# Kernel tuning notes

Hardware: AMD Instinct MI355X
Metric: run time of the kernel (lower is better)

Reference implementation:

```python
import jax, jax.numpy as jnp
import numpy as np

D_IN = 1024
D_OUT = 1024
NUM_HEADS = 16
HEAD_DIM = D_OUT // NUM_HEADS


def setup_inputs() -> dict:
    key = jax.random.key(0)
    k1, k2, k3, k4 = jax.random.split(key, 4)
    x = jax.random.normal(k1, (2, 2048, D_IN), dtype=jnp.float32)
    # qkv Linear (bias=False): weight [3*d_out, d_in]
    w_qkv = jax.random.normal(k2, (3 * D_OUT, D_IN), dtype=jnp.float32) * (1.0 / np.sqrt(D_IN))
    # proj Linear (default bias=True): weight [d_out, d_out], bias [d_out]
    w_proj = jax.random.normal(k3, (D_OUT, D_OUT), dtype=jnp.float32) * (1.0 / np.sqrt(D_OUT))
    b_proj = jax.random.normal(k4, (D_OUT,), dtype=jnp.float32) * 0.01
    return {"x": x, "w_qkv": w_qkv, "w_proj": w_proj, "b_proj": b_proj}


def reference(x, w_qkv, w_proj, b_proj):
    B, S, E = x.shape
    qkv = jnp.einsum("bse,fe->bsf", x, w_qkv)                 # [B,S,3*d_out]
    qkv = qkv.reshape(B, S, 3, NUM_HEADS, HEAD_DIM)
    qkv = jnp.transpose(qkv, (2, 0, 3, 1, 4))                  # [3,B,H,S,D]
    q, k, v = qkv[0], qkv[1], qkv[2]
    scores = jnp.einsum("bhqd,bhkd->bhqk", q, k)               # [B,H,S,S]
    causal = jnp.triu(jnp.ones((S, S), dtype=bool), k=1)
    scores = jnp.where(causal, -jnp.inf, scores)
    # NOTE: source divides by head_dim**(-0.5), i.e. multiplies by sqrt(head_dim)
    scores = scores / (HEAD_DIM ** -0.5)
    attn = jax.nn.softmax(scores, axis=-1)
    ctx = jnp.einsum("bhqk,bhkd->bhqd", attn, v)               # [B,H,S,D]
    ctx = jnp.transpose(ctx, (0, 2, 1, 3)).reshape(B, S, E)
    return jnp.einsum("bse,fe->bsf", ctx, w_proj) + b_proj
```

## Files before the change

### kernel.cpp

```cpp
#include <hip/hip_runtime.h>

typedef _Float16 f16;
typedef _Float16 f16x4 __attribute__((ext_vector_type(4)));
typedef _Float16 f16x8 __attribute__((ext_vector_type(8)));
typedef float f32x4 __attribute__((ext_vector_type(4)));

#define MFMA16(a, b, c) __builtin_amdgcn_mfma_f32_16x16x32_f16(a, b, c, 0, 0, 0)
#define QSCALE 11.5415603f

typedef const __attribute__((address_space(1))) void* gp1_t;
typedef __attribute__((address_space(3))) void* lp3_t;
__device__ __forceinline__ void gld16(const void* g, void* l) {
    __builtin_amdgcn_global_load_lds((gp1_t)g, (lp3_t)l, 16, 0, 0);
}

__global__ __launch_bounds__(256) void cvt_all(
    const float* __restrict__ x, const float* __restrict__ wq, const float* __restrict__ wp,
    f16* __restrict__ xh, f16* __restrict__ wqh, f16* __restrict__ wph)
{
    int i = blockIdx.x * 256 + threadIdx.x;
    const float4* src; f16x4* dst; int off;
    if (i < 1048576)      { src = (const float4*)x;  dst = (f16x4*)xh;  off = i; }
    else if (i < 1835008) { src = (const float4*)wq; dst = (f16x4*)wqh; off = i - 1048576; }
    else                  { src = (const float4*)wp; dst = (f16x4*)wph; off = i - 1835008; }
    float4 v = src[off];
    f16x4 o = { (f16)v.x, (f16)v.y, (f16)v.z, (f16)v.w };
    dst[off] = o;
}

template<int EPI>
__global__ __launch_bounds__(256) void gemm_k(
    const f16* __restrict__ A, const f16* __restrict__ B, int K,
    f16* __restrict__ qb, f16* __restrict__ kb, f16* __restrict__ vt,
    float* __restrict__ outF, const float* __restrict__ bias)
{
    __shared__ f16 as[128 * 32];
    __shared__ f16 bs[128 * 32];
    const int t = threadIdx.x;
    const int m0 = blockIdx.y * 128, n0 = blockIdx.x * 128;
    const int lane = t & 63, wv = t >> 6;
    const int wm = wv >> 1, wn = wv & 1;
    const int lr = lane & 15, g = lane >> 4;
    const int srow = lane >> 2, schk = (lane & 3) * 8;
    const f16* Ab = A + (size_t)m0 * K;
    const f16* Bb = B + (size_t)n0 * K;
    f32x4 acc[4][4] = {};

    for (int k0 = 0; k0 < K; k0 += 32) {
        __syncthreads();
        #pragma unroll
        for (int i2 = 0; i2 < 2; ++i2) {
            const int r0 = wv * 32 + i2 * 16;
            gld16(&Ab[(size_t)(r0 + srow) * K + k0 + schk], &as[r0 * 32]);
            gld16(&Bb[(size_t)(r0 + srow) * K + k0 + schk], &bs[r0 * 32]);
        }
        __syncthreads();
        f16x8 af[4], bf[4];
        #pragma unroll
        for (int mt = 0; mt < 4; ++mt)
            af[mt] = *reinterpret_cast<const f16x8*>(&as[(wm * 64 + mt * 16 + lr) * 32 + g * 8]);
        #pragma unroll
        for (int nt = 0; nt < 4; ++nt)
            bf[nt] = *reinterpret_cast<const f16x8*>(&bs[(wn * 64 + nt * 16 + lr) * 32 + g * 8]);
        #pragma unroll
        for (int mt = 0; mt < 4; ++mt)
            #pragma unroll
            for (int nt = 0; nt < 4; ++nt)
                acc[mt][nt] = MFMA16(af[mt], bf[nt], acc[mt][nt]);
    }

    #pragma unroll
    for (int mt = 0; mt < 4; ++mt) {
        #pragma unroll
        for (int nt = 0; nt < 4; ++nt) {
            const int n = n0 + wn * 64 + nt * 16 + lr;
            const int s0 = m0 + wm * 64 + mt * 16 + 4 * g;
            if (EPI == 0) {
                const int which = n >> 10, h = (n >> 6) & 15, d = n & 63;
                const int b = s0 >> 11, s = s0 & 2047;
                if (which == 2) {
                    f16x4 vv;
                    #pragma unroll
                    for (int i = 0; i < 4; ++i) vv[i] = (f16)acc[mt][nt][i];
                    *reinterpret_cast<f16x4*>(&vt[((size_t)((b << 4) + h) * 64 + d) * 2048 + s]) = vv;
                } else {
                    f16* dst = which ? kb : qb;
                    const float sc = which ? 1.0f : QSCALE;
                    #pragma unroll
                    for (int i = 0; i < 4; ++i)
                        dst[((size_t)((b << 4) + h) * 2048 + (s + i)) * 64 + d] = (f16)(acc[mt][nt][i] * sc);
                }
            } else {
                #pragma unroll
                for (int i = 0; i < 4; ++i)
                    outF[(size_t)(s0 + i) * 1024 + n] = acc[mt][nt][i] + bias[n];
            }
        }
    }
}

__global__ __launch_bounds__(64, 2) void attn_k(
    const f16* __restrict__ Q, const f16* __restrict__ K, const f16* __restrict__ VT,
    f16* __restrict__ ctx, f16* __restrict__ opart,
    float* __restrict__ mpart, float* __restrict__ lpart)
{
    __shared__ f16 lp[64][72];
    const int lane = threadIdx.x;
    const int lr = lane & 15, g = lane >> 4;
    const int bid = blockIdx.x;
    const int bh = bid & 31;
    const int rr = 67 - (bid >> 5);
    int u, c;
    if (rr < 10)      { u = rr;                 c = 0; }
    else if (rr < 30) { u = 10 + (rr - 10) / 2; c = (rr - 10) % 2; }
    else if (rr < 60) { u = 20 + (rr - 30) / 3; c = (rr - 30) % 3; }
    else              { u = 30 + (rr - 60) / 4; c = (rr - 60) % 4; }
    const int ntt = u + 1;
    const int nc  = 1 + u / 10;
    const int cbase = ntt / nc, crem = ntt % nc;
    const int start = c * cbase + (c < crem ? c : crem);
    const int len   = cbase + (c < crem ? 1 : 0);
    const bool diag = (start + len == ntt);

    const int b = bh >> 4, h = bh & 15;
    const size_t base = (size_t)bh * (2048 * 64);
    const f16* Qb = Q + base;
    const f16* Kb = K + base;
    const f16* Vb = VT + base;
    const int q0 = u << 6;

    f16x8 qf[4][2];
    #pragma unroll
    for (int nt = 0; nt < 4; ++nt)
        #pragma unroll
        for (int ks = 0; ks < 2; ++ks)
            qf[nt][ks] = *reinterpret_cast<const f16x8*>(&Qb[(size_t)(q0 + nt * 16 + lr) * 64 + ks * 32 + g * 8]);

    f32x4 o[4][4] = {};
    float mrun[4] = { -1e30f, -1e30f, -1e30f, -1e30f };
    float lsum[4] = { 0.f, 0.f, 0.f, 0.f };

#define ATTN_TILE(KV0, DIAGM) do {                                                      \
    const int kv0_ = (KV0);                                                             \
    f32x4 st[4][4] = {};                                                                \
    _Pragma("unroll")                                                                   \
    for (int mt = 0; mt < 4; ++mt) {                                                    \
        f16x8 ak[2];                                                                    \
        _Pragma("unroll")                                                               \
        for (int ks = 0; ks < 2; ++ks)                                                  \
            ak[ks] = *reinterpret_cast<const f16x8*>(                                   \
                &Kb[(size_t)(kv0_ + mt * 16 + lr) * 64 + ks * 32 + g * 8]);             \
        _Pragma("unroll")                                                               \
        for (int nt = 0; nt < 4; ++nt)                                                  \
            if (!(DIAGM) || mt <= nt) {                                                 \
                _Pragma("unroll")                                                       \
                for (int ks = 0; ks < 2; ++ks)                                          \
                    st[mt][nt] = MFMA16(ak[ks], qf[nt][ks], st[mt][nt]);                \
            }                                                                           \
    }                                                                                   \
    _Pragma("unroll")                                                                   \
    for (int nt = 0; nt < 4; ++nt) {                                                    \
        float mloc = -1e30f;                                                            \
        _Pragma("unroll")                                                               \
        for (int mt = 0; mt < 4; ++mt) {                                                \
            if ((DIAGM) && mt > nt) continue;                                           \
            _Pragma("unroll")                                                           \
            for (int i = 0; i < 4; ++i) {                                               \
                float sv = st[mt][nt][i];                                               \
                if ((DIAGM) && mt == nt) {             \
                    sv = (4 * g + i <= lr) ? sv : -1e30f;                               \
                    st[mt][nt][i] = sv;                                                 \
                }                                                                       \
                mloc = fmaxf(mloc, sv);                                                 \
            }                                                                           \
        }                                                                               \
        mloc = fmaxf(mloc, __shfl_xor(mloc, 16));                                       \
        mloc = fmaxf(mloc, __shfl_xor(mloc, 32));                                       \
        if (__any(mloc > mrun[nt] + 8.0f)) {                             \
            float mnew = fmaxf(mrun[nt], mloc);                                         \
            float sc = exp2f(mrun[nt] - mnew);                                          \
            lsum[nt] *= sc;                                                             \
            _Pragma("unroll")                                                           \
            for (int mo = 0; mo < 4; ++mo)                                              \
                _Pragma("unroll")                                                       \
                for (int i = 0; i < 4; ++i) o[mo][nt][i] *= sc;                         \
            mrun[nt] = mnew;                                                            \
        }                                                                               \
        float ls = 0.f;                                                                 \
        _Pragma("unroll")                                                               \
        for (int mt = 0; mt < 4; ++mt) {                                                \
            f16x4 pk;                                                                   \
            if ((DIAGM) && mt > nt) {                                                   \
                pk[0] = pk[1] = pk[2] = pk[3] = (f16)0.f;                               \
            } else {                                                                    \
                _Pragma("unroll")                                                       \
                for (int i = 0; i < 4; ++i) {                                           \
                    float p = exp2f(st[mt][nt][i] - mrun[nt]);                          \
                    ls += p; pk[i] = (f16)p;                                            \
                }                                                                       \
            }                                                                           \
            *reinterpret_cast<f16x4*>(&lp[nt * 16 + lr][mt * 16 + 4 * g]) = pk;         \
        }                                                                               \
        lsum[nt] += ls;                                                                 \
    }                                                                                   \
    {                                                                                   \
        f16x8 pf[4][2];                                                                 \
        _Pragma("unroll")                                                               \
        for (int nt = 0; nt < 4; ++nt)                                                  \
            _Pragma("unroll")                                                           \
            for (int ks = 0; ks < 2; ++ks)                                              \
                pf[nt][ks] = *reinterpret_cast<const f16x8*>(                           \
                    &lp[nt * 16 + lr][ks * 32 + g * 8]);                                \
        _Pragma("unroll")                                                               \
        for (int mo = 0; mo < 4; ++mo) {                                                \
            f16x8 av[2];                                                                \
            _Pragma("unroll")                                                           \
            for (int ks = 0; ks < 2; ++ks)                                              \
                av[ks] = *reinterpret_cast<const f16x8*>(                               \
                    &Vb[(size_t)(mo * 16 + lr) * 2048 + kv0_ + ks * 32 + g * 8]);       \
            _Pragma("unroll")                                                           \
            for (int nt = 0; nt < 4; ++nt)                                              \
                _Pragma("unroll")                                                       \
                for (int ks = 0; ks < 2; ++ks)                                          \
                    o[mo][nt] = MFMA16(av[ks], pf[nt][ks], o[mo][nt]);                  \
        }                                                                               \
    }                                                                                   \
} while (0)

    const int tEnd = start + len - (diag ? 1 : 0);
    for (int tt = start; tt < tEnd; ++tt)
        ATTN_TILE(tt << 6, 0);
    if (diag)
        ATTN_TILE((ntt - 1) << 6, 1);
#undef ATTN_TILE

    const bool split = (nc > 1);
    int slot = 0;
    if (split) {
        const int psl = (u < 20) ? 2 * (u - 10) : (u < 30 ? 20 + 3 * (u - 20) : 50 + 4 * (u - 30));
        slot = bh * 58 + psl + c;
    }
    #pragma unroll
    for (int nt = 0; nt < 4; ++nt) {
        float l = lsum[nt];
        l += __shfl_xor(l, 16);
        l += __shfl_xor(l, 32);
        const float inv = 1.0f / l;
        const int lrow = nt * 16 + lr;
        if (!split) {
            const size_t rowoff = ((size_t)(b * 2048 + q0 + lrow)) * 1024 + h * 64;
            #pragma unroll
            for (int mo = 0; mo < 4; ++mo) {
                f16x4 ov;
                #pragma unroll
                for (int i = 0; i < 4; ++i) ov[i] = (f16)(o[mo][nt][i] * inv);
                *reinterpret_cast<f16x4*>(&ctx[rowoff + mo * 16 + 4 * g]) = ov;
            }
        } else {
            const int mi = slot * 64 + lrow;
            #pragma unroll
            for (int mo = 0; mo < 4; ++mo) {
                f16x4 ov;
                #pragma unroll
                for (int i = 0; i < 4; ++i) ov[i] = (f16)(o[mo][nt][i] * inv);
                *reinterpret_cast<f16x4*>(&opart[(size_t)mi * 64 + mo * 16 + 4 * g]) = ov;
            }
            if (g == 0) { mpart[mi] = mrun[nt]; lpart[mi] = l; }
        }
    }
}

__global__ __launch_bounds__(256) void combine_k(
    const f16* __restrict__ opart, const float* __restrict__ mpart,
    const float* __restrict__ lpart, f16* __restrict__ ctx)
{
    const int blk = blockIdx.x;
    const int bh = blk & 31, u = 10 + (blk >> 5);
    const int b = bh >> 4, h = bh & 15;
    const int nc = 1 + u / 10;
    const int psl = (u < 20) ? 2 * (u - 10) : (u < 30 ? 20 + 3 * (u - 20) : 50 + 4 * (u - 30));
    const int slot0 = bh * 58 + psl;
    const int t = threadIdx.x;
    const int lrow = t >> 2, seg = t & 3;

    float m[4], l[4], w[4];
    float M = -1e30f;
    #pragma unroll 4
    for (int cc = 0; cc < 4; ++cc) if (cc < nc) {
        m[cc] = mpart[(slot0 + cc) * 64 + lrow];
        l[cc] = lpart[(slot0 + cc) * 64 + lrow];
        M = fmaxf(M, m[cc]);
    }
    float wsum = 0.f;
    #pragma unroll 4
    for (int cc = 0; cc < 4; ++cc) if (cc < nc) { w[cc] = l[cc] * exp2f(m[cc] - M); wsum += w[cc]; }
    const float r = 1.0f / wsum;

    float acc[16] = {};
    #pragma unroll 4
    for (int cc = 0; cc < 4; ++cc) if (cc < nc) {
        const float coef = w[cc] * r;
        const size_t rb = (size_t)((slot0 + cc) * 64 + lrow) * 64 + seg * 16;
        f16x8 v0 = *reinterpret_cast<const f16x8*>(&opart[rb]);
        f16x8 v1 = *reinterpret_cast<const f16x8*>(&opart[rb + 8]);
        #pragma unroll
        for (int i = 0; i < 8; ++i) { acc[i] += coef * (float)v0[i]; acc[i + 8] += coef * (float)v1[i]; }
    }
    f16x8 o0, o1;
    #pragma unroll
    for (int i = 0; i < 8; ++i) { o0[i] = (f16)acc[i]; o1[i] = (f16)acc[i + 8]; }
    const size_t wb = ((size_t)(b * 2048 + u * 64 + lrow)) * 1024 + h * 64 + seg * 16;
    *reinterpret_cast<f16x8*>(&ctx[wb]) = o0;
    *reinterpret_cast<f16x8*>(&ctx[wb + 8]) = o1;
}

extern "C" void kernel_launch(void* const* d_in, const int* in_sizes, int n_in,
                              void* d_out, int out_size, void* d_ws, size_t ws_size,
                              hipStream_t stream) {
    const float* x      = (const float*)d_in[0];
    const float* w_qkv  = (const float*)d_in[1];
    const float* w_proj = (const float*)d_in[2];
    const float* b_proj = (const float*)d_in[3];
    float* out = (float*)d_out;

    char* p = (char*)d_ws;
    f16* xh     = (f16*)p; p += (size_t)4096 * 1024 * 2;
    f16* wqkvh  = (f16*)p; p += (size_t)3072 * 1024 * 2;
    f16* wprojh = (f16*)p; p += (size_t)1024 * 1024 * 2;
    f16* qbuf   = (f16*)p; p += (size_t)2 * 16 * 2048 * 64 * 2;
    f16* kbuf   = (f16*)p; p += (size_t)2 * 16 * 2048 * 64 * 2;
    f16* vtbuf  = (f16*)p; p += (size_t)2 * 16 * 64 * 2048 * 2;
    f16* ctx    = (f16*)p; p += (size_t)4096 * 1024 * 2;

    f16*   opart = (f16*)d_out;
    float* mpart = (float*)xh;
    float* lpart = mpart + 118784;

    cvt_all<<<8192, 256, 0, stream>>>(x, w_qkv, w_proj, xh, wqkvh, wprojh);

    gemm_k<0><<<dim3(24, 32), 256, 0, stream>>>(xh, wqkvh, 1024, qbuf, kbuf, vtbuf, nullptr, nullptr);

    attn_k<<<2176, 64, 0, stream>>>(qbuf, kbuf, vtbuf, ctx, opart, mpart, lpart);

    combine_k<<<704, 256, 0, stream>>>(opart, mpart, lpart, ctx);

    gemm_k<1><<<dim3(8, 32), 256, 0, stream>>>(ctx, wprojh, 1024, nullptr, nullptr, nullptr, out, b_proj);
}
```

Measured before the change: 199.5 us.

## Double-buffer K fragments in attention, swizzle GEMM blocks, narrow proj GEMM tile

The attention loop now prefetches the next K tile into a second register buffer while computing on the current one, so global K-load latency is hidden behind MFMA work. The GEMM kernel gains an N-tile template parameter and a block-index swizzle that groups blocks for better L2 reuse. The output projection switches to a 64-wide N tile with twice as many blocks to fill more compute units. The costs are extra VGPRs for the double buffer, which may reduce occupancy, and less data reuse per block in the proj GEMM.

```diff
diff --git a/kernel.cpp b/kernel.cpp
--- a/kernel.cpp
+++ b/kernel.cpp
@@ -28,23 +28,28 @@
     dst[off] = o;
 }
 
-template<int EPI>
+template<int EPI, int BN>
 __global__ __launch_bounds__(256) void gemm_k(
     const f16* __restrict__ A, const f16* __restrict__ B, int K,
     f16* __restrict__ qb, f16* __restrict__ kb, f16* __restrict__ vt,
     float* __restrict__ outF, const float* __restrict__ bias)
 {
     __shared__ f16 as[128 * 32];
-    __shared__ f16 bs[128 * 32];
+    __shared__ f16 bs[BN * 32];
+    constexpr int WN = BN / 2;
+    constexpr int NT = BN / 32;
     const int t = threadIdx.x;
-    const int m0 = blockIdx.y * 128, n0 = blockIdx.x * 128;
+    const int bidf = blockIdx.y * gridDim.x + blockIdx.x;
+    const int cpx  = (gridDim.x * gridDim.y) >> 3;
+    const int swz  = (bidf & 7) * cpx + (bidf >> 3);
+    const int m0 = (swz / gridDim.x) * 128, n0 = (swz % gridDim.x) * BN;
     const int lane = t & 63, wv = t >> 6;
     const int wm = wv >> 1, wn = wv & 1;
     const int lr = lane & 15, g = lane >> 4;
     const int srow = lane >> 2, schk = (lane & 3) * 8;
     const f16* Ab = A + (size_t)m0 * K;
     const f16* Bb = B + (size_t)n0 * K;
-    f32x4 acc[4][4] = {};
+    f32x4 acc[4][NT] = {};
 
     for (int k0 = 0; k0 < K; k0 += 32) {
         __syncthreads();
@@ -52,28 +57,37 @@
         for (int i2 = 0; i2 < 2; ++i2) {
             const int r0 = wv * 32 + i2 * 16;
             gld16(&Ab[(size_t)(r0 + srow) * K + k0 + schk], &as[r0 * 32]);
+        }
+        if constexpr (BN == 128) {
+            #pragma unroll
+            for (int i2 = 0; i2 < 2; ++i2) {
+                const int r0 = wv * 32 + i2 * 16;
+                gld16(&Bb[(size_t)(r0 + srow) * K + k0 + schk], &bs[r0 * 32]);
+            }
+        } else {
+            const int r0 = wv * 16;
             gld16(&Bb[(size_t)(r0 + srow) * K + k0 + schk], &bs[r0 * 32]);
         }
         __syncthreads();
-        f16x8 af[4], bf[4];
+        f16x8 af[4], bf[NT];
         #pragma unroll
         for (int mt = 0; mt < 4; ++mt)
             af[mt] = *reinterpret_cast<const f16x8*>(&as[(wm * 64 + mt * 16 + lr) * 32 + g * 8]);
         #pragma unroll
-        for (int nt = 0; nt < 4; ++nt)
-            bf[nt] = *reinterpret_cast<const f16x8*>(&bs[(wn * 64 + nt * 16 + lr) * 32 + g * 8]);
+        for (int nt = 0; nt < NT; ++nt)
+            bf[nt] = *reinterpret_cast<const f16x8*>(&bs[(wn * WN + nt * 16 + lr) * 32 + g * 8]);
         #pragma unroll
         for (int mt = 0; mt < 4; ++mt)
             #pragma unroll
-            for (int nt = 0; nt < 4; ++nt)
+            for (int nt = 0; nt < NT; ++nt)
                 acc[mt][nt] = MFMA16(af[mt], bf[nt], acc[mt][nt]);
     }
 
     #pragma unroll
     for (int mt = 0; mt < 4; ++mt) {
         #pragma unroll
-        for (int nt = 0; nt < 4; ++nt) {
-            const int n = n0 + wn * 64 + nt * 16 + lr;
+        for (int nt = 0; nt < NT; ++nt) {
+            const int n = n0 + wn * WN + nt * 16 + lr;
             const int s0 = m0 + wm * 64 + mt * 16 + 4 * g;
             if (EPI == 0) {
                 const int which = n >> 10, h = (n >> 6) & 15, d = n & 63;
@@ -139,25 +153,30 @@
     f32x4 o[4][4] = {};
     float mrun[4] = { -1e30f, -1e30f, -1e30f, -1e30f };
     float lsum[4] = { 0.f, 0.f, 0.f, 0.f };
-
-#define ATTN_TILE(KV0, DIAGM) do {                                                      \
-    const int kv0_ = (KV0);                                                             \
+    f16x8 akA[4][2], akB[4][2];
+
+#define LOADK(BUF, I) do {                                                              \
+    const int kvL_ = (start + (I)) << 6;                                                \
+    _Pragma("unroll")                                                                   \
+    for (int mt = 0; mt < 4; ++mt)                                                      \
+        _Pragma("unroll")                                                               \
+        for (int ks = 0; ks < 2; ++ks)                                                  \
+            BUF[mt][ks] = *reinterpret_cast<const f16x8*>(                              \
+                &Kb[(size_t)(kvL_ + mt * 16 + lr) * 64 + ks * 32 + g * 8]);             \
+} while (0)
+
+#define TILE_BODY(BUF, I, DIAGM) do {                                                   \
+    const int kv0_ = (start + (I)) << 6;                                                \
     f32x4 st[4][4] = {};                                                                \
     _Pragma("unroll")                                                                   \
-    for (int mt = 0; mt < 4; ++mt) {                                                    \
-        f16x8 ak[2];                                                                    \
-        _Pragma("unroll")                                                               \
-        for (int ks = 0; ks < 2; ++ks)                                                  \
-            ak[ks] = *reinterpret_cast<const f16x8*>(                                   \
-                &Kb[(size_t)(kv0_ + mt * 16 + lr) * 64 + ks * 32 + g * 8]);             \
+    for (int mt = 0; mt < 4; ++mt)                                                      \
         _Pragma("unroll")                                                               \
         for (int nt = 0; nt < 4; ++nt)                                                  \
             if (!(DIAGM) || mt <= nt) {                                                 \
                 _Pragma("unroll")                                                       \
                 for (int ks = 0; ks < 2; ++ks)                                          \
-                    st[mt][nt] = MFMA16(ak[ks], qf[nt][ks], st[mt][nt]);                \
+                    st[mt][nt] = MFMA16(BUF[mt][ks], qf[nt][ks], st[mt][nt]);           \
             }                                                                           \
-    }                                                                                   \
     _Pragma("unroll")                                                                   \
     for (int nt = 0; nt < 4; ++nt) {                                                    \
         float mloc = -1e30f;                                                            \
@@ -167,7 +186,7 @@
             _Pragma("unroll")                                                           \
             for (int i = 0; i < 4; ++i) {                                               \
                 float sv = st[mt][nt][i];                                               \
-                if ((DIAGM) && mt == nt) {             \
+                if ((DIAGM) && mt == nt) {         \
                     sv = (4 * g + i <= lr) ? sv : -1e30f;                               \
                     st[mt][nt][i] = sv;                                                 \
                 }                                                                       \
@@ -227,12 +246,28 @@
     }                                                                                   \
 } while (0)
 
-    const int tEnd = start + len - (diag ? 1 : 0);
-    for (int tt = start; tt < tEnd; ++tt)
-        ATTN_TILE(tt << 6, 0);
-    if (diag)
-        ATTN_TILE((ntt - 1) << 6, 1);
-#undef ATTN_TILE
+    const int nfull = len - (diag ? 1 : 0);
+    LOADK(akA, 0);
+    int i = 0;
+    for (; i + 2 <= nfull; i += 2) {
+        LOADK(akB, i + 1);
+        TILE_BODY(akA, i, 0);
+        if (i + 2 < len) LOADK(akA, i + 2);
+        TILE_BODY(akB, i + 1, 0);
+    }
+    if (i < nfull) {
+        if (diag) {
+            LOADK(akB, i + 1);
+            TILE_BODY(akA, i, 0);
+            TILE_BODY(akB, i + 1, 1);
+        } else {
+            TILE_BODY(akA, i, 0);
+        }
+    } else if (diag) {
+        TILE_BODY(akA, nfull, 1);
+    }
+#undef LOADK
+#undef TILE_BODY
 
     const bool split = (nc > 1);
     int slot = 0;
@@ -253,7 +288,7 @@
             for (int mo = 0; mo < 4; ++mo) {
                 f16x4 ov;
                 #pragma unroll
-                for (int i = 0; i < 4; ++i) ov[i] = (f16)(o[mo][nt][i] * inv);
+                for (int i2 = 0; i2 < 4; ++i2) ov[i2] = (f16)(o[mo][nt][i2] * inv);
                 *reinterpret_cast<f16x4*>(&ctx[rowoff + mo * 16 + 4 * g]) = ov;
             }
         } else {
@@ -262,7 +297,7 @@
             for (int mo = 0; mo < 4; ++mo) {
                 f16x4 ov;
                 #pragma unroll
-                for (int i = 0; i < 4; ++i) ov[i] = (f16)(o[mo][nt][i] * inv);
+                for (int i2 = 0; i2 < 4; ++i2) ov[i2] = (f16)(o[mo][nt][i2] * inv);
                 *reinterpret_cast<f16x4*>(&opart[(size_t)mi * 64 + mo * 16 + 4 * g]) = ov;
             }
             if (g == 0) { mpart[mi] = mrun[nt]; lpart[mi] = l; }
@@ -338,11 +373,11 @@
 
     cvt_all<<<8192, 256, 0, stream>>>(x, w_qkv, w_proj, xh, wqkvh, wprojh);
 
-    gemm_k<0><<<dim3(24, 32), 256, 0, stream>>>(xh, wqkvh, 1024, qbuf, kbuf, vtbuf, nullptr, nullptr);
+    gemm_k<0, 128><<<dim3(24, 32), 256, 0, stream>>>(xh, wqkvh, 1024, qbuf, kbuf, vtbuf, nullptr, nullptr);
 
     attn_k<<<2176, 64, 0, stream>>>(qbuf, kbuf, vtbuf, ctx, opart, mpart, lpart);
 
     combine_k<<<704, 256, 0, stream>>>(opart, mpart, lpart, ctx);
 
-    gemm_k<1><<<dim3(8, 32), 256, 0, stream>>>(ctx, wprojh, 1024, nullptr, nullptr, nullptr, out, b_proj);
-}
+    gemm_k<1, 64><<<dim3(16, 32), 256, 0, stream>>>(ctx, wprojh, 1024, nullptr, nullptr, nullptr, out, b_proj);
+}
```

After: 196.4 us. No clear change (-1.5%).
